# Kernel optimization log

Measured on AMD Instinct MI355X. Metric: run time of the kernel, lower is better.

The kernel has to match this reference:

```python
import jax, jax.numpy as jnp
import numpy as np

N = 100000   # nodes
E = 1600000  # edges (avg degree 16)
D = 128      # input feature dim
H = 64       # hidden dim (hard-coded in Sage.__init__)
C = 40       # output classes


def setup_inputs() -> dict:
    key = jax.random.key(0)
    ks = jax.random.split(key, 9)
    s_in = 1.0 / np.sqrt(D)
    s_h = 1.0 / np.sqrt(H)
    return {
        "x": jax.random.normal(ks[0], (N, D), jnp.float32),
        "edge_index": jax.random.randint(ks[1], (2, E), 0, N, dtype=jnp.int64),
        # SAGEConv params: lin_l acts on aggregated neighbors (carries bias),
        # lin_r acts on the root/self features (no bias), per PyG defaults.
        "W1_l": jax.random.uniform(ks[2], (D, H), jnp.float32, -s_in, s_in),
        "W1_r": jax.random.uniform(ks[3], (D, H), jnp.float32, -s_in, s_in),
        "b1": jax.random.uniform(ks[4], (H,), jnp.float32, -s_in, s_in),
        "W2_l": jax.random.uniform(ks[5], (H, C), jnp.float32, -s_h, s_h),
        "W2_r": jax.random.uniform(ks[6], (H, C), jnp.float32, -s_h, s_h),
        "b2": jax.random.uniform(ks[7], (C,), jnp.float32, -s_h, s_h),
    }


def _sage_conv(x, src, dst, W_l, W_r, b):
    # mean-aggregate neighbor features at destination nodes
    msg = x[src]                                             # [E, F] gather
    summed = jax.ops.segment_sum(msg, dst, num_segments=N)   # [N, F]
    deg = jax.ops.segment_sum(jnp.ones((src.shape[0],), x.dtype), dst,
                              num_segments=N)                # [N]
    agg = summed / jnp.maximum(deg, 1.0)[:, None]
    return agg @ W_l + x @ W_r + b


def reference(x, edge_index, W1_l, W1_r, b1, W2_l, W2_r, b2):
    src, dst = edge_index[0], edge_index[1]
    h = _sage_conv(x, src, dst, W1_l, W1_r, b1)
    h = jax.nn.relu(h)
    # F.dropout(training=False) in eval mode -> identity
    out = _sage_conv(h, src, dst, W2_l, W2_r, b2)
    return jax.nn.log_softmax(out, axis=1)
```

## Files before the change

### kernel.cpp

```cpp
#include <hip/hip_runtime.h>

__device__ __forceinline__ float bf2f(unsigned short u) {
  union { unsigned int i; float f; } c; c.i = ((unsigned int)u) << 16; return c.f;
}
__device__ __forceinline__ unsigned short f2bf(float f) {
  union { float f; unsigned int i; } c; c.f = f;
  unsigned int x = c.i;
  return (unsigned short)((x + 0x7fffu + ((x >> 16) & 1u)) >> 16);
}
__device__ __forceinline__ float lo16(unsigned int w) { return bf2f((unsigned short)(w & 0xffffu)); }
__device__ __forceinline__ float hi16(unsigned int w) { return bf2f((unsigned short)(w >> 16)); }

#define DD 128
#define HH 64
#define CC 40
#define NBUCK 256
#define NCHUNK 128
#define MAXNPB 512
#define NQ 4
#define NR 4

using bf16x8 = __attribute__((ext_vector_type(8))) short;
using f32x4  = __attribute__((ext_vector_type(4))) float;

__global__ __launch_bounds__(256) void detect(const unsigned int* e32,
                                              const unsigned int* x32, int* flags) {
  __shared__ unsigned int redOr[256];
  __shared__ int redCnt[256];
  int tid = threadIdx.x;
  unsigned int v = 0;
  for (int i = tid; i < 4096; i += 256) v |= e32[2 * i + 1];
  int cnt = 0;
  for (int i = tid; i < 4096; i += 256) {
    unsigned int w = x32[i];
    unsigned int expo = (w >> 7) & 0xffu;
    unsigned short lo = (unsigned short)(w & 0xffffu);
    if (lo == 0 || (expo >= 100u && expo <= 133u)) cnt++;
  }
  redOr[tid] = v; redCnt[tid] = cnt; __syncthreads();
  for (int s = 128; s > 0; s >>= 1) {
    if (tid < s) { redOr[tid] |= redOr[tid + s]; redCnt[tid] += redCnt[tid + s]; }
    __syncthreads();
  }
  if (tid == 0) {
    flags[0] = (redOr[0] == 0u) ? 1 : 0;
    flags[1] = (redCnt[0] < 2048) ? 1 : 0;
  }
}

__global__ __launch_bounds__(256) void hist_k(const int* e32, int E, int N,
                                              const int* flags, int nodesPerB,
                                              int* histG) {
  __shared__ int cnt[NBUCK * NR];
  int tid = threadIdx.x;
  for (int i = tid; i < NBUCK * NR; i += 256) cnt[i] = 0;
  __syncthreads();
  int isI64 = flags[0];
  int rep = tid & (NR - 1);
  int chunk = (E + NCHUNK - 1) / NCHUNK;
  int e0 = blockIdx.x * chunk, e1 = min(e0 + chunk, E);
  for (int i = e0 + tid; i < e1; i += 256) {
    int d = isI64 ? e32[2 * (E + i)] : e32[E + i];
    d = min(max(d, 0), N - 1);
    atomicAdd(&cnt[(d / nodesPerB) * NR + rep], 1);
  }
  __syncthreads();
  for (int i = tid; i < NBUCK; i += 256)
    histG[i * NCHUNK + blockIdx.x] =
        cnt[i * NR] + cnt[i * NR + 1] + cnt[i * NR + 2] + cnt[i * NR + 3];
}

__global__ __launch_bounds__(128) void scanA(const int* histG, int* ohist, int* bsum) {
  __shared__ int t[NCHUNK];
  int b = blockIdx.x, tid = threadIdx.x;
  int v = histG[b * NCHUNK + tid];
  t[tid] = v; __syncthreads();
  for (int st = 1; st < NCHUNK; st <<= 1) {
    int u = (tid >= st) ? t[tid - st] : 0;
    __syncthreads();
    t[tid] += u;
    __syncthreads();
  }
  ohist[b * NCHUNK + tid] = t[tid] - v;
  if (tid == NCHUNK - 1) bsum[b] = t[tid];
}

__global__ __launch_bounds__(256) void scanB_prepw(const int* bsum, int* bbase,
                                                   int* row_ptr4, int N, int E,
                                                   const void* W1l, const void* W1r,
                                                   const void* b1,
                                                   const void* W2l, const void* W2r,
                                                   const void* b2,
                                                   const int* flags,
                                                   unsigned short* Wb1,
                                                   unsigned short* Wb2,
                                                   float* b1f, float* b2f) {
  int tid = threadIdx.x;
  if (blockIdx.x == 1) {
    int isf = flags[1];
    auto rd = [&](const void* p, int i) -> float {
      return isf ? ((const float*)p)[i] : bf2f(((const unsigned short*)p)[i]);
    };
    for (int idx = tid; idx < 128 * 128; idx += 256) {
      int n = idx >> 7, k = idx & 127;
      float v = (n < HH) ? rd(W1l, k * HH + n) : rd(W1r, k * HH + (n - HH));
      Wb1[idx] = f2bf(v);
    }
    for (int idx = tid; idx < 48 * 128; idx += 256) {
      int n = idx >> 7, k = idx & 127;
      float v = 0.f;
      if (n < CC) v = (k < HH) ? rd(W2l, k * CC + n) : rd(W2r, (k - HH) * CC + n);
      Wb2[idx] = f2bf(v);
    }
    if (tid < HH) b1f[tid] = rd(b1, tid);
    if (tid < CC) b2f[tid] = rd(b2, tid);
    return;
  }
  __shared__ int t[NBUCK];
  int v = bsum[tid];
  t[tid] = v; __syncthreads();
  for (int st = 1; st < NBUCK; st <<= 1) {
    int u = (tid >= st) ? t[tid - st] : 0;
    __syncthreads();
    t[tid] += u;
    __syncthreads();
  }
  bbase[tid] = t[tid] - v;
  if (tid == 0) { bbase[NBUCK] = E; row_ptr4[NQ * N] = E; }
}

__global__ __launch_bounds__(256) void scatter_k(const int* e32, int E, int N,
                                                 const int* flags, int nodesPerB,
                                                 const int* ohist, const int* bbase,
                                                 uint2* ebuf) {
  __shared__ int cur[NBUCK];
  int tid = threadIdx.x;
  if (tid < NBUCK) cur[tid] = ohist[tid * NCHUNK + blockIdx.x] + bbase[tid];
  __syncthreads();
  int isI64 = flags[0];
  int chunk = (E + NCHUNK - 1) / NCHUNK;
  int e0 = blockIdx.x * chunk, e1 = min(e0 + chunk, E);
  for (int i = e0 + tid; i < e1; i += 256) {
    int s, d;
    if (isI64) { s = e32[2 * i]; d = e32[2 * (E + i)]; }
    else       { s = e32[i];     d = e32[E + i]; }
    s = min(max(s, 0), N - 1);
    d = min(max(d, 0), N - 1);
    int p = atomicAdd(&cur[d / nodesPerB], 1);
    ebuf[p] = make_uint2((unsigned)s, (unsigned)d);
  }
}

__global__ __launch_bounds__(256) void bktB_or_t1(
    const uint2* ebuf, const int* bbase,
    int nbuck, int nodesPerB, int qshift, int* row_ptr4, float* invd, int* col, int N,
    const void* xraw, const int* flags, const unsigned short* Wb1, const float* b1f,
    unsigned short* t1, unsigned short* s1, int T1B) {
  __shared__ int ldsb[MAXNPB * NQ + 256];
  int b = blockIdx.x;
  int tid = threadIdx.x;

  if (b < nbuck) {
    int* cnt = ldsb;
    int* sA  = ldsb + MAXNPB * NQ;
    int base_node = b * nodesPerB;
    int nn = min(nodesPerB, N - base_node);
    if (nn <= 0) return;
    int nk = nn * NQ;
    int eb0 = bbase[b], eb1 = bbase[b + 1];
    int nE = eb1 - eb0;
    const uint2* ee = ebuf + eb0;
    for (int i = tid; i < nk; i += 256) cnt[i] = 0;
    __syncthreads();
    for (int i = tid; i < nE; i += 256) {
      uint2 eg = ee[i];
      int key = ((int)eg.y - base_node) * NQ + (int)(eg.x >> qshift);
      atomicAdd(&cnt[key], 1);
    }
    __syncthreads();
    for (int i = tid; i < nn; i += 256) {
      int d = cnt[NQ * i] + cnt[NQ * i + 1] + cnt[NQ * i + 2] + cnt[NQ * i + 3];
      invd[base_node + i] = 1.0f / (float)max(d, 1);
    }
    __syncthreads();
    int per = (nk + 255) / 256;
    int myb = tid * per;
    int dreg[8];
    int ssum = 0;
#pragma unroll
    for (int k = 0; k < 8; k++) {
      int idx = myb + k;
      int v = (k < per && idx < nk) ? cnt[idx] : 0;
      dreg[k] = v; ssum += v;
    }
    sA[tid] = ssum;
    __syncthreads();
    for (int st = 1; st < 256; st <<= 1) {
      int t = (tid >= st) ? sA[tid - st] : 0;
      __syncthreads();
      sA[tid] += t;
      __syncthreads();
    }
    int run = eb0 + sA[tid] - ssum;
    __syncthreads();
#pragma unroll
    for (int k = 0; k < 8; k++) {
      int idx = myb + k;
      if (k < per && idx < nk) {
        row_ptr4[(size_t)(base_node + (idx >> 2)) * NQ + (idx & 3)] = run;
        cnt[idx] = run;
        run += dreg[k];
      }
    }
    __syncthreads();
    for (int i = tid; i < nE; i += 256) {
      uint2 eg = ee[i];
      int key = ((int)eg.y - base_node) * NQ + (int)(eg.x >> qshift);
      int p = atomicAdd(&cnt[key], 1);
      col[p] = (int)eg.x;
    }
    return;
  }

  int t = b - nbuck;
  if (t >= T1B) return;
  int lane = tid & 63, wv = tid >> 6;
  int nb = t * 64 + wv * 16;
  int oc = lane & 15, kgrp = lane >> 4;
  int node = min(nb + oc, N - 1);
  f32x4 acc[8];
#pragma unroll
  for (int i = 0; i < 8; i++) acc[i] = (f32x4){0.f, 0.f, 0.f, 0.f};

  if (flags[1]) {
    const float4* x4 = (const float4*)xraw;
#pragma unroll
    for (int kb = 0; kb < 4; kb++) {
      int k0 = kb * 32 + kgrp * 8;
      float4 a0 = x4[(size_t)node * 32 + (k0 >> 2)];
      float4 a1 = x4[(size_t)node * 32 + (k0 >> 2) + 1];
      bf16x8 af;
      af[0] = (short)f2bf(a0.x); af[1] = (short)f2bf(a0.y);
      af[2] = (short)f2bf(a0.z); af[3] = (short)f2bf(a0.w);
      af[4] = (short)f2bf(a1.x); af[5] = (short)f2bf(a1.y);
      af[6] = (short)f2bf(a1.z); af[7] = (short)f2bf(a1.w);
#pragma unroll
      for (int nblk = 0; nblk < 8; nblk++) {
        bf16x8 bfr = *(const bf16x8*)&Wb1[(nblk * 16 + oc) * 128 + k0];
        acc[nblk] = __builtin_amdgcn_mfma_f32_16x16x32_bf16(af, bfr, acc[nblk], 0, 0, 0);
      }
    }
  } else {
    const unsigned short* x16 = (const unsigned short*)xraw;
#pragma unroll
    for (int kb = 0; kb < 4; kb++) {
      int k0 = kb * 32 + kgrp * 8;
      bf16x8 af = *(const bf16x8*)&x16[(size_t)node * 128 + k0];
#pragma unroll
      for (int nblk = 0; nblk < 8; nblk++) {
        bf16x8 bfr = *(const bf16x8*)&Wb1[(nblk * 16 + oc) * 128 + k0];
        acc[nblk] = __builtin_amdgcn_mfma_f32_16x16x32_bf16(af, bfr, acc[nblk], 0, 0, 0);
      }
    }
  }

  int r0 = kgrp * 4;
#pragma unroll
  for (int nblk = 0; nblk < 8; nblk++) {
    float bias = (nblk >= 4) ? b1f[(nblk - 4) * 16 + oc] : 0.f;
#pragma unroll
    for (int r = 0; r < 4; r++) {
      int nn = nb + r0 + r;
      if (nn < N) {
        if (nblk < 4)
          t1[(size_t)nn * HH + nblk * 16 + oc] = f2bf(acc[nblk][r]);
        else
          s1[(size_t)nn * HH + (nblk - 4) * 16 + oc] = f2bf(acc[nblk][r] + bias);
      }
    }
  }
}

__device__ __forceinline__ void gather_seg(const uint4* t8, const int* col,
                                           int s0, int s1, int r, int c,
                                           float acc[8]) {
  for (int base = s0; base < s1; base += 4) {
    int i = base + r;
    bool g = (i < s1);
    int nb = g ? col[i] : 0;
    uint4 v = make_uint4(0, 0, 0, 0);
    if (g) v = t8[(size_t)nb * 8 + c];
    acc[0] += lo16(v.x); acc[1] += hi16(v.x);
    acc[2] += lo16(v.y); acc[3] += hi16(v.y);
    acc[4] += lo16(v.z); acc[5] += hi16(v.z);
    acc[6] += lo16(v.w); acc[7] += hi16(v.w);
  }
}

__global__ __launch_bounds__(256) void aggregate1(const unsigned short* t1,
                                                  const unsigned short* s1,
                                                  const int* row_ptr4, const float* invd,
                                                  const int* col, unsigned short* h, int N) {
  int wave = threadIdx.x >> 6, lane = threadIdx.x & 63;
  int ns = lane >> 5, r = (lane >> 3) & 3, c = lane & 7;
  int n = blockIdx.x * 8 + wave * 2 + ns;
  if (n >= N) return;
  int4 rp = *(const int4*)&row_ptr4[(size_t)NQ * n];
  int e4 = row_ptr4[(size_t)NQ * n + 4];
  float acc[8] = {0, 0, 0, 0, 0, 0, 0, 0};
  const uint4* t8 = (const uint4*)t1;
  gather_seg(t8, col, rp.x, rp.y, r, c, acc);
  gather_seg(t8, col, rp.y, rp.z, r, c, acc);
  gather_seg(t8, col, rp.z, rp.w, r, c, acc);
  gather_seg(t8, col, rp.w, e4, r, c, acc);
#pragma unroll
  for (int m = 8; m <= 16; m <<= 1)
#pragma unroll
    for (int i = 0; i < 8; i++) acc[i] += __shfl_xor(acc[i], m, 64);

  if (r == 0) {
    float id = invd[n];
    uint4 sv = ((const uint4*)s1)[(size_t)n * 8 + c];
    float s[8] = {lo16(sv.x), hi16(sv.x), lo16(sv.y), hi16(sv.y),
                  lo16(sv.z), hi16(sv.z), lo16(sv.w), hi16(sv.w)};
    unsigned int o[4];
#pragma unroll
    for (int i = 0; i < 4; i++) {
      float a0 = fmaxf(acc[2 * i] * id + s[2 * i], 0.f);
      float a1 = fmaxf(acc[2 * i + 1] * id + s[2 * i + 1], 0.f);
      o[i] = (unsigned int)f2bf(a0) | ((unsigned int)f2bf(a1) << 16);
    }
    ((uint4*)h)[(size_t)n * 8 + c] = make_uint4(o[0], o[1], o[2], o[3]);
  }
}

__global__ __launch_bounds__(256) void agg2(const unsigned short* h,
                                            const int* row_ptr4, const float* invd,
                                            const int* col, unsigned short* aggh, int N) {
  int wave = threadIdx.x >> 6, lane = threadIdx.x & 63;
  int ns = lane >> 5, r = (lane >> 3) & 3, c = lane & 7;
  int n = blockIdx.x * 8 + wave * 2 + ns;
  if (n >= N) return;
  int4 rp = *(const int4*)&row_ptr4[(size_t)NQ * n];
  int e4 = row_ptr4[(size_t)NQ * n + 4];
  float acc[8] = {0, 0, 0, 0, 0, 0, 0, 0};
  const uint4* h8 = (const uint4*)h;
  gather_seg(h8, col, rp.x, rp.y, r, c, acc);
  gather_seg(h8, col, rp.y, rp.z, r, c, acc);
  gather_seg(h8, col, rp.z, rp.w, r, c, acc);
  gather_seg(h8, col, rp.w, e4, r, c, acc);
#pragma unroll
  for (int m = 8; m <= 16; m <<= 1)
#pragma unroll
    for (int i = 0; i < 8; i++) acc[i] += __shfl_xor(acc[i], m, 64);

  if (r == 0) {
    float id = invd[n];
    unsigned int o[4];
#pragma unroll
    for (int i = 0; i < 4; i++) {
      o[i] = (unsigned int)f2bf(acc[2 * i] * id) |
             ((unsigned int)f2bf(acc[2 * i + 1] * id) << 16);
    }
    ((uint4*)aggh)[(size_t)n * 8 + c] = make_uint4(o[0], o[1], o[2], o[3]);
  }
}

__global__ __launch_bounds__(256) void final_k(const unsigned short* aggh,
                                               const unsigned short* h,
                                               const unsigned short* Wb2,
                                               const float* b2f,
                                               float* out, int N) {
  int tid = threadIdx.x;
  int lane = tid & 63, wv = tid >> 6;
  int nb = blockIdx.x * 64 + wv * 16;
  int oc = lane & 15, kgrp = lane >> 4;
  int node = min(nb + oc, N - 1);
  f32x4 acc[3];
#pragma unroll
  for (int i = 0; i < 3; i++) acc[i] = (f32x4){0.f, 0.f, 0.f, 0.f};

#pragma unroll
  for (int kb = 0; kb < 4; kb++) {
    int k0 = kb * 32 + kgrp * 8;
    const unsigned short* src = (kb < 2) ? aggh : h;
    int kk = k0 & 63;
    bf16x8 af = *(const bf16x8*)&src[(size_t)node * HH + kk];
#pragma unroll
    for (int nblk = 0; nblk < 3; nblk++) {
      bf16x8 bfr = *(const bf16x8*)&Wb2[(nblk * 16 + oc) * 128 + k0];
      acc[nblk] = __builtin_amdgcn_mfma_f32_16x16x32_bf16(af, bfr, acc[nblk], 0, 0, 0);
    }
  }

#pragma unroll
  for (int nblk = 0; nblk < 3; nblk++) {
    int cc = nblk * 16 + oc;
    float bias = (cc < CC) ? b2f[cc] : 0.f;
#pragma unroll
    for (int r = 0; r < 4; r++) acc[nblk][r] += bias;
  }

#pragma unroll
  for (int r = 0; r < 4; r++) {
    int nn = nb + kgrp * 4 + r;
    float m = -INFINITY;
#pragma unroll
    for (int nblk = 0; nblk < 3; nblk++)
      if (nblk * 16 + oc < CC) m = fmaxf(m, acc[nblk][r]);
    for (int off = 1; off <= 8; off <<= 1) m = fmaxf(m, __shfl_xor(m, off, 64));
    float s = 0.f;
#pragma unroll
    for (int nblk = 0; nblk < 3; nblk++)
      if (nblk * 16 + oc < CC) s += __expf(acc[nblk][r] - m);
    for (int off = 1; off <= 8; off <<= 1) s += __shfl_xor(s, off, 64);
    float lse = m + __logf(s);
    if (nn < N) {
#pragma unroll
      for (int nblk = 0; nblk < 3; nblk++) {
        int cc = nblk * 16 + oc;
        if (cc < CC) out[(size_t)nn * CC + cc] = acc[nblk][r] - lse;
      }
    }
  }
}

extern "C" void kernel_launch(void* const* d_in, const int* in_sizes, int n_in,
                              void* d_out, int out_size, void* d_ws, size_t ws_size,
                              hipStream_t stream) {
  const void* x   = d_in[0];
  const int*  e   = (const int*)d_in[1];
  const void* W1l = d_in[2];
  const void* W1r = d_in[3];
  const void* b1  = d_in[4];
  const void* W2l = d_in[5];
  const void* W2r = d_in[6];
  const void* b2  = d_in[7];
  float* out = (float*)d_out;

  const int N = in_sizes[0] / DD;
  const int E = in_sizes[1] / 2;
  const int nodesPerB = (N + NBUCK - 1) / NBUCK;
  const int nbuck = (N + nodesPerB - 1) / nodesPerB;
  const int T1B = (N + 63) / 64;
  int qshift = 0;
  while (((unsigned)(N - 1) >> qshift) > 3u) qshift++;

  char* w = (char*)d_ws;
  size_t off = 0;
  auto carve = [&](size_t bytes) -> void* {
    void* p = (void*)(w + off);
    off += (bytes + 255) & ~(size_t)255;
    return p;
  };
  int* col      = (int*)carve((size_t)E * 4);
  int* row_ptr4 = (int*)carve(((size_t)N * NQ + 1) * 4);
  float* invd   = (float*)carve((size_t)N * 4);
  int* histG    = (int*)carve((size_t)NBUCK * NCHUNK * 4);
  int* ohist    = (int*)carve((size_t)NBUCK * NCHUNK * 4);
  int* bsum     = (int*)carve(NBUCK * 4);
  int* bbase    = (int*)carve((NBUCK + 1) * 4);
  int* flags    = (int*)carve(8);
  unsigned short* t1   = (unsigned short*)carve((size_t)N * HH * 2);
  unsigned short* s1   = (unsigned short*)carve((size_t)N * HH * 2);
  unsigned short* h    = (unsigned short*)carve((size_t)N * HH * 2);
  unsigned short* Wb1  = (unsigned short*)carve(128 * 128 * 2);
  unsigned short* Wb2  = (unsigned short*)carve(48 * 128 * 2);
  float* b1f   = (float*)carve(HH * sizeof(float));
  float* b2f   = (float*)carve(CC * sizeof(float));
  uint2* ebuf  = (uint2*)carve((size_t)E * 8);
  unsigned short* aggh = (unsigned short*)ebuf;
  (void)ws_size; (void)n_in; (void)out_size;

  detect<<<1, 256, 0, stream>>>((const unsigned int*)e, (const unsigned int*)x, flags);
  hist_k<<<NCHUNK, 256, 0, stream>>>(e, E, N, flags, nodesPerB, histG);
  scanA<<<NBUCK, 128, 0, stream>>>(histG, ohist, bsum);
  scanB_prepw<<<2, 256, 0, stream>>>(bsum, bbase, row_ptr4, N, E,
                                     W1l, W1r, b1, W2l, W2r, b2,
                                     flags, Wb1, Wb2, b1f, b2f);
  scatter_k<<<NCHUNK, 256, 0, stream>>>(e, E, N, flags, nodesPerB, ohist, bbase, ebuf);
  bktB_or_t1<<<nbuck + T1B, 256, 0, stream>>>(ebuf, bbase,
                                              nbuck, nodesPerB, qshift, row_ptr4,
                                              invd, col, N,
                                              x, flags, Wb1, b1f, t1, s1, T1B);
  aggregate1<<<(N + 7) / 8, 256, 0, stream>>>(t1, s1, row_ptr4, invd, col, h, N);
  agg2<<<(N + 7) / 8, 256, 0, stream>>>(h, row_ptr4, invd, col, aggh, N);
  final_k<<<(N + 63) / 64, 256, 0, stream>>>(aggh, h, Wb2, b2f, out, N);
}
```

Measured before the change: 328.6 us.

## Reschedule layer-1 transform into histogram kernel and double bucket count

Weight preparation moves into the detect kernel, spread across extra blocks, and the layer-1 MFMA transform now runs alongside the edge histogram rather than alongside the bucket CSR build. NBUCK doubles to 512 and MAXNPB halves, so each bucket block covers fewer nodes and there are more of them, which should improve load balance and LDS use in bktB. scanB is now a standalone single block of 512 threads. The weight blocks re-detect the input dtype from W1l rather than from x. This heuristic could disagree with the flag computed by block 0, and scanA now launches twice as many blocks.

```diff
diff --git a/kernel.cpp b/kernel.cpp
--- a/kernel.cpp
+++ b/kernel.cpp
@@ -14,60 +14,164 @@
 #define DD 128
 #define HH 64
 #define CC 40
-#define NBUCK 256
+#define NBUCK 512
 #define NCHUNK 128
-#define MAXNPB 512
+#define MAXNPB 256
 #define NQ 4
 #define NR 4
 
 using bf16x8 = __attribute__((ext_vector_type(8))) short;
 using f32x4  = __attribute__((ext_vector_type(4))) float;
 
-__global__ __launch_bounds__(256) void detect(const unsigned int* e32,
-                                              const unsigned int* x32, int* flags) {
-  __shared__ unsigned int redOr[256];
-  __shared__ int redCnt[256];
+__global__ __launch_bounds__(256) void detect_prepw(
+    const unsigned int* e32, const unsigned int* x32, int* flags,
+    const void* W1l, const void* W1r, const void* b1,
+    const void* W2l, const void* W2r, const void* b2,
+    unsigned short* Wb1, unsigned short* Wb2, float* b1f, float* b2f) {
   int tid = threadIdx.x;
-  unsigned int v = 0;
-  for (int i = tid; i < 4096; i += 256) v |= e32[2 * i + 1];
+  if (blockIdx.x == 0) {
+    __shared__ unsigned int redOr[256];
+    __shared__ int redCnt[256];
+    unsigned int v = 0;
+    for (int i = tid; i < 4096; i += 256) v |= e32[2 * i + 1];
+    int cnt = 0;
+    for (int i = tid; i < 4096; i += 256) {
+      unsigned int w = x32[i];
+      unsigned int expo = (w >> 7) & 0xffu;
+      unsigned short lo = (unsigned short)(w & 0xffffu);
+      if (lo == 0 || (expo >= 100u && expo <= 133u)) cnt++;
+    }
+    redOr[tid] = v; redCnt[tid] = cnt; __syncthreads();
+    for (int s = 128; s > 0; s >>= 1) {
+      if (tid < s) { redOr[tid] |= redOr[tid + s]; redCnt[tid] += redCnt[tid + s]; }
+      __syncthreads();
+    }
+    if (tid == 0) {
+      flags[0] = (redOr[0] == 0u) ? 1 : 0;
+      flags[1] = (redCnt[0] < 2048) ? 1 : 0;
+    }
+    return;
+  }
+  __shared__ int red[256];
+  const unsigned int* w32 = (const unsigned int*)W1l;
   int cnt = 0;
   for (int i = tid; i < 4096; i += 256) {
-    unsigned int w = x32[i];
+    unsigned int w = w32[i];
     unsigned int expo = (w >> 7) & 0xffu;
     unsigned short lo = (unsigned short)(w & 0xffffu);
     if (lo == 0 || (expo >= 100u && expo <= 133u)) cnt++;
   }
-  redOr[tid] = v; redCnt[tid] = cnt; __syncthreads();
+  red[tid] = cnt; __syncthreads();
   for (int s = 128; s > 0; s >>= 1) {
-    if (tid < s) { redOr[tid] |= redOr[tid + s]; redCnt[tid] += redCnt[tid + s]; }
-    __syncthreads();
-  }
-  if (tid == 0) {
-    flags[0] = (redOr[0] == 0u) ? 1 : 0;
-    flags[1] = (redCnt[0] < 2048) ? 1 : 0;
-  }
-}
-
-__global__ __launch_bounds__(256) void hist_k(const int* e32, int E, int N,
-                                              const int* flags, int nodesPerB,
-                                              int* histG) {
+    if (tid < s) red[tid] += red[tid + s];
+    __syncthreads();
+  }
+  int isf = (red[0] < 2048) ? 1 : 0;
+  auto rd = [&](const void* p, int i) -> float {
+    return isf ? ((const float*)p)[i] : bf2f(((const unsigned short*)p)[i]);
+  };
+  if (blockIdx.x == 1) {
+    for (int idx = tid; idx < 128 * 128; idx += 256) {
+      int n = idx >> 7, k = idx & 127;
+      float v = (n < HH) ? rd(W1l, k * HH + n) : rd(W1r, k * HH + (n - HH));
+      Wb1[idx] = f2bf(v);
+    }
+  } else {
+    for (int idx = tid; idx < 48 * 128; idx += 256) {
+      int n = idx >> 7, k = idx & 127;
+      float v = 0.f;
+      if (n < CC) v = (k < HH) ? rd(W2l, k * CC + n) : rd(W2r, (k - HH) * CC + n);
+      Wb2[idx] = f2bf(v);
+    }
+    if (tid < HH) b1f[tid] = rd(b1, tid);
+    if (tid < CC) b2f[tid] = rd(b2, tid);
+  }
+}
+
+__global__ __launch_bounds__(256) void hist_or_t1(
+    const int* e32, int E, int N, const int* flags, int nodesPerB, int* histG,
+    const void* xraw, const unsigned short* Wb1, const float* b1f,
+    unsigned short* t1, unsigned short* s1, int T1B) {
   __shared__ int cnt[NBUCK * NR];
+  int b = blockIdx.x;
   int tid = threadIdx.x;
-  for (int i = tid; i < NBUCK * NR; i += 256) cnt[i] = 0;
-  __syncthreads();
-  int isI64 = flags[0];
-  int rep = tid & (NR - 1);
-  int chunk = (E + NCHUNK - 1) / NCHUNK;
-  int e0 = blockIdx.x * chunk, e1 = min(e0 + chunk, E);
-  for (int i = e0 + tid; i < e1; i += 256) {
-    int d = isI64 ? e32[2 * (E + i)] : e32[E + i];
-    d = min(max(d, 0), N - 1);
-    atomicAdd(&cnt[(d / nodesPerB) * NR + rep], 1);
-  }
-  __syncthreads();
-  for (int i = tid; i < NBUCK; i += 256)
-    histG[i * NCHUNK + blockIdx.x] =
-        cnt[i * NR] + cnt[i * NR + 1] + cnt[i * NR + 2] + cnt[i * NR + 3];
+
+  if (b < NCHUNK) {
+    for (int i = tid; i < NBUCK * NR; i += 256) cnt[i] = 0;
+    __syncthreads();
+    int isI64 = flags[0];
+    int rep = tid & (NR - 1);
+    int chunk = (E + NCHUNK - 1) / NCHUNK;
+    int e0 = b * chunk, e1 = min(e0 + chunk, E);
+    for (int i = e0 + tid; i < e1; i += 256) {
+      int d = isI64 ? e32[2 * (E + i)] : e32[E + i];
+      d = min(max(d, 0), N - 1);
+      atomicAdd(&cnt[(d / nodesPerB) * NR + rep], 1);
+    }
+    __syncthreads();
+    for (int i = tid; i < NBUCK; i += 256)
+      histG[i * NCHUNK + b] =
+          cnt[i * NR] + cnt[i * NR + 1] + cnt[i * NR + 2] + cnt[i * NR + 3];
+    return;
+  }
+
+  int t = b - NCHUNK;
+  if (t >= T1B) return;
+  int lane = tid & 63, wv = tid >> 6;
+  int nb = t * 64 + wv * 16;
+  int oc = lane & 15, kgrp = lane >> 4;
+  int node = min(nb + oc, N - 1);
+  f32x4 acc[8];
+#pragma unroll
+  for (int i = 0; i < 8; i++) acc[i] = (f32x4){0.f, 0.f, 0.f, 0.f};
+
+  if (flags[1]) {
+    const float4* x4 = (const float4*)xraw;
+#pragma unroll
+    for (int kb = 0; kb < 4; kb++) {
+      int k0 = kb * 32 + kgrp * 8;
+      float4 a0 = x4[(size_t)node * 32 + (k0 >> 2)];
+      float4 a1 = x4[(size_t)node * 32 + (k0 >> 2) + 1];
+      bf16x8 af;
+      af[0] = (short)f2bf(a0.x); af[1] = (short)f2bf(a0.y);
+      af[2] = (short)f2bf(a0.z); af[3] = (short)f2bf(a0.w);
+      af[4] = (short)f2bf(a1.x); af[5] = (short)f2bf(a1.y);
+      af[6] = (short)f2bf(a1.z); af[7] = (short)f2bf(a1.w);
+#pragma unroll
+      for (int nblk = 0; nblk < 8; nblk++) {
+        bf16x8 bfr = *(const bf16x8*)&Wb1[(nblk * 16 + oc) * 128 + k0];
+        acc[nblk] = __builtin_amdgcn_mfma_f32_16x16x32_bf16(af, bfr, acc[nblk], 0, 0, 0);
+      }
+    }
+  } else {
+    const unsigned short* x16 = (const unsigned short*)xraw;
+#pragma unroll
+    for (int kb = 0; kb < 4; kb++) {
+      int k0 = kb * 32 + kgrp * 8;
+      bf16x8 af = *(const bf16x8*)&x16[(size_t)node * 128 + k0];
+#pragma unroll
+      for (int nblk = 0; nblk < 8; nblk++) {
+        bf16x8 bfr = *(const bf16x8*)&Wb1[(nblk * 16 + oc) * 128 + k0];
+        acc[nblk] = __builtin_amdgcn_mfma_f32_16x16x32_bf16(af, bfr, acc[nblk], 0, 0, 0);
+      }
+    }
+  }
+
+  int r0 = kgrp * 4;
+#pragma unroll
+  for (int nblk = 0; nblk < 8; nblk++) {
+    float bias = (nblk >= 4) ? b1f[(nblk - 4) * 16 + oc] : 0.f;
+#pragma unroll
+    for (int r = 0; r < 4; r++) {
+      int nn = nb + r0 + r;
+      if (nn < N) {
+        if (nblk < 4)
+          t1[(size_t)nn * HH + nblk * 16 + oc] = f2bf(acc[nblk][r]);
+        else
+          s1[(size_t)nn * HH + (nblk - 4) * 16 + oc] = f2bf(acc[nblk][r] + bias);
+      }
+    }
+  }
 }
 
 __global__ __launch_bounds__(128) void scanA(const int* histG, int* ohist, int* bsum) {
@@ -85,38 +189,10 @@
   if (tid == NCHUNK - 1) bsum[b] = t[tid];
 }
 
-__global__ __launch_bounds__(256) void scanB_prepw(const int* bsum, int* bbase,
-                                                   int* row_ptr4, int N, int E,
-                                                   const void* W1l, const void* W1r,
-                                                   const void* b1,
-                                                   const void* W2l, const void* W2r,
-                                                   const void* b2,
-                                                   const int* flags,
-                                                   unsigned short* Wb1,
-                                                   unsigned short* Wb2,
-                                                   float* b1f, float* b2f) {
+__global__ __launch_bounds__(512) void scanB(const int* bsum, int* bbase,
+                                             int* row_ptr4, int N, int E) {
+  __shared__ int t[NBUCK];
   int tid = threadIdx.x;
-  if (blockIdx.x == 1) {
-    int isf = flags[1];
-    auto rd = [&](const void* p, int i) -> float {
-      return isf ? ((const float*)p)[i] : bf2f(((const unsigned short*)p)[i]);
-    };
-    for (int idx = tid; idx < 128 * 128; idx += 256) {
-      int n = idx >> 7, k = idx & 127;
-      float v = (n < HH) ? rd(W1l, k * HH + n) : rd(W1r, k * HH + (n - HH));
-      Wb1[idx] = f2bf(v);
-    }
-    for (int idx = tid; idx < 48 * 128; idx += 256) {
-      int n = idx >> 7, k = idx & 127;
-      float v = 0.f;
-      if (n < CC) v = (k < HH) ? rd(W2l, k * CC + n) : rd(W2r, (k - HH) * CC + n);
-      Wb2[idx] = f2bf(v);
-    }
-    if (tid < HH) b1f[tid] = rd(b1, tid);
-    if (tid < CC) b2f[tid] = rd(b2, tid);
-    return;
-  }
-  __shared__ int t[NBUCK];
   int v = bsum[tid];
   t[tid] = v; __syncthreads();
   for (int st = 1; st < NBUCK; st <<= 1) {
@@ -135,7 +211,8 @@
                                                  uint2* ebuf) {
   __shared__ int cur[NBUCK];
   int tid = threadIdx.x;
-  if (tid < NBUCK) cur[tid] = ohist[tid * NCHUNK + blockIdx.x] + bbase[tid];
+  for (int i = tid; i < NBUCK; i += 256)
+    cur[i] = ohist[i * NCHUNK + blockIdx.x] + bbase[i];
   __syncthreads();
   int isI64 = flags[0];
   int chunk = (E + NCHUNK - 1) / NCHUNK;
@@ -151,133 +228,68 @@
   }
 }
 
-__global__ __launch_bounds__(256) void bktB_or_t1(
+__global__ __launch_bounds__(256) void bktB(
     const uint2* ebuf, const int* bbase,
-    int nbuck, int nodesPerB, int qshift, int* row_ptr4, float* invd, int* col, int N,
-    const void* xraw, const int* flags, const unsigned short* Wb1, const float* b1f,
-    unsigned short* t1, unsigned short* s1, int T1B) {
-  __shared__ int ldsb[MAXNPB * NQ + 256];
+    int nodesPerB, int qshift, int* row_ptr4, float* invd, int* col, int N) {
+  __shared__ int cnt[MAXNPB * NQ];
+  __shared__ int sA[256];
   int b = blockIdx.x;
   int tid = threadIdx.x;
-
-  if (b < nbuck) {
-    int* cnt = ldsb;
-    int* sA  = ldsb + MAXNPB * NQ;
-    int base_node = b * nodesPerB;
-    int nn = min(nodesPerB, N - base_node);
-    if (nn <= 0) return;
-    int nk = nn * NQ;
-    int eb0 = bbase[b], eb1 = bbase[b + 1];
-    int nE = eb1 - eb0;
-    const uint2* ee = ebuf + eb0;
-    for (int i = tid; i < nk; i += 256) cnt[i] = 0;
-    __syncthreads();
-    for (int i = tid; i < nE; i += 256) {
-      uint2 eg = ee[i];
-      int key = ((int)eg.y - base_node) * NQ + (int)(eg.x >> qshift);
-      atomicAdd(&cnt[key], 1);
-    }
-    __syncthreads();
-    for (int i = tid; i < nn; i += 256) {
-      int d = cnt[NQ * i] + cnt[NQ * i + 1] + cnt[NQ * i + 2] + cnt[NQ * i + 3];
-      invd[base_node + i] = 1.0f / (float)max(d, 1);
-    }
-    __syncthreads();
-    int per = (nk + 255) / 256;
-    int myb = tid * per;
-    int dreg[8];
-    int ssum = 0;
-#pragma unroll
-    for (int k = 0; k < 8; k++) {
-      int idx = myb + k;
-      int v = (k < per && idx < nk) ? cnt[idx] : 0;
-      dreg[k] = v; ssum += v;
-    }
-    sA[tid] = ssum;
-    __syncthreads();
-    for (int st = 1; st < 256; st <<= 1) {
-      int t = (tid >= st) ? sA[tid - st] : 0;
-      __syncthreads();
-      sA[tid] += t;
-      __syncthreads();
-    }
-    int run = eb0 + sA[tid] - ssum;
-    __syncthreads();
-#pragma unroll
-    for (int k = 0; k < 8; k++) {
-      int idx = myb + k;
-      if (k < per && idx < nk) {
-        row_ptr4[(size_t)(base_node + (idx >> 2)) * NQ + (idx & 3)] = run;
-        cnt[idx] = run;
-        run += dreg[k];
-      }
-    }
-    __syncthreads();
-    for (int i = tid; i < nE; i += 256) {
-      uint2 eg = ee[i];
-      int key = ((int)eg.y - base_node) * NQ + (int)(eg.x >> qshift);
-      int p = atomicAdd(&cnt[key], 1);
-      col[p] = (int)eg.x;
-    }
-    return;
-  }
-
-  int t = b - nbuck;
-  if (t >= T1B) return;
-  int lane = tid & 63, wv = tid >> 6;
-  int nb = t * 64 + wv * 16;
-  int oc = lane & 15, kgrp = lane >> 4;
-  int node = min(nb + oc, N - 1);
-  f32x4 acc[8];
-#pragma unroll
-  for (int i = 0; i < 8; i++) acc[i] = (f32x4){0.f, 0.f, 0.f, 0.f};
-
-  if (flags[1]) {
-    const float4* x4 = (const float4*)xraw;
-#pragma unroll
-    for (int kb = 0; kb < 4; kb++) {
-      int k0 = kb * 32 + kgrp * 8;
-      float4 a0 = x4[(size_t)node * 32 + (k0 >> 2)];
-      float4 a1 = x4[(size_t)node * 32 + (k0 >> 2) + 1];
-      bf16x8 af;
-      af[0] = (short)f2bf(a0.x); af[1] = (short)f2bf(a0.y);
-      af[2] = (short)f2bf(a0.z); af[3] = (short)f2bf(a0.w);
-      af[4] = (short)f2bf(a1.x); af[5] = (short)f2bf(a1.y);
-      af[6] = (short)f2bf(a1.z); af[7] = (short)f2bf(a1.w);
-#pragma unroll
-      for (int nblk = 0; nblk < 8; nblk++) {
-        bf16x8 bfr = *(const bf16x8*)&Wb1[(nblk * 16 + oc) * 128 + k0];
-        acc[nblk] = __builtin_amdgcn_mfma_f32_16x16x32_bf16(af, bfr, acc[nblk], 0, 0, 0);
-      }
-    }
-  } else {
-    const unsigned short* x16 = (const unsigned short*)xraw;
-#pragma unroll
-    for (int kb = 0; kb < 4; kb++) {
-      int k0 = kb * 32 + kgrp * 8;
-      bf16x8 af = *(const bf16x8*)&x16[(size_t)node * 128 + k0];
-#pragma unroll
-      for (int nblk = 0; nblk < 8; nblk++) {
-        bf16x8 bfr = *(const bf16x8*)&Wb1[(nblk * 16 + oc) * 128 + k0];
-        acc[nblk] = __builtin_amdgcn_mfma_f32_16x16x32_bf16(af, bfr, acc[nblk], 0, 0, 0);
-      }
-    }
-  }
-
-  int r0 = kgrp * 4;
-#pragma unroll
-  for (int nblk = 0; nblk < 8; nblk++) {
-    float bias = (nblk >= 4) ? b1f[(nblk - 4) * 16 + oc] : 0.f;
-#pragma unroll
-    for (int r = 0; r < 4; r++) {
-      int nn = nb + r0 + r;
-      if (nn < N) {
-        if (nblk < 4)
-          t1[(size_t)nn * HH + nblk * 16 + oc] = f2bf(acc[nblk][r]);
-        else
-          s1[(size_t)nn * HH + (nblk - 4) * 16 + oc] = f2bf(acc[nblk][r] + bias);
-      }
-    }
+  int base_node = b * nodesPerB;
+  int nn = min(nodesPerB, N - base_node);
+  if (nn <= 0) return;
+  int nk = nn * NQ;
+  int eb0 = bbase[b], eb1 = bbase[b + 1];
+  int nE = eb1 - eb0;
+  const uint2* ee = ebuf + eb0;
+  for (int i = tid; i < nk; i += 256) cnt[i] = 0;
+  __syncthreads();
+  for (int i = tid; i < nE; i += 256) {
+    uint2 eg = ee[i];
+    int key = ((int)eg.y - base_node) * NQ + (int)(eg.x >> qshift);
+    atomicAdd(&cnt[key], 1);
+  }
+  __syncthreads();
+  for (int i = tid; i < nn; i += 256) {
+    int d = cnt[NQ * i] + cnt[NQ * i + 1] + cnt[NQ * i + 2] + cnt[NQ * i + 3];
+    invd[base_node + i] = 1.0f / (float)max(d, 1);
+  }
+  __syncthreads();
+  int per = (nk + 255) / 256;
+  int myb = tid * per;
+  int dreg[4];
+  int ssum = 0;
+#pragma unroll
+  for (int k = 0; k < 4; k++) {
+    int idx = myb + k;
+    int v = (k < per && idx < nk) ? cnt[idx] : 0;
+    dreg[k] = v; ssum += v;
+  }
+  sA[tid] = ssum;
+  __syncthreads();
+  for (int st = 1; st < 256; st <<= 1) {
+    int t = (tid >= st) ? sA[tid - st] : 0;
+    __syncthreads();
+    sA[tid] += t;
+    __syncthreads();
+  }
+  int run = eb0 + sA[tid] - ssum;
+  __syncthreads();
+#pragma unroll
+  for (int k = 0; k < 4; k++) {
+    int idx = myb + k;
+    if (k < per && idx < nk) {
+      row_ptr4[(size_t)(base_node + (idx >> 2)) * NQ + (idx & 3)] = run;
+      cnt[idx] = run;
+      run += dreg[k];
+    }
+  }
+  __syncthreads();
+  for (int i = tid; i < nE; i += 256) {
+    uint2 eg = ee[i];
+    int key = ((int)eg.y - base_node) * NQ + (int)(eg.x >> qshift);
+    int p = atomicAdd(&cnt[key], 1);
+    col[p] = (int)eg.x;
   }
 }
 
@@ -472,17 +484,16 @@
   unsigned short* aggh = (unsigned short*)ebuf;
   (void)ws_size; (void)n_in; (void)out_size;
 
-  detect<<<1, 256, 0, stream>>>((const unsigned int*)e, (const unsigned int*)x, flags);
-  hist_k<<<NCHUNK, 256, 0, stream>>>(e, E, N, flags, nodesPerB, histG);
+  detect_prepw<<<3, 256, 0, stream>>>((const unsigned int*)e, (const unsigned int*)x,
+                                      flags, W1l, W1r, b1, W2l, W2r, b2,
+                                      Wb1, Wb2, b1f, b2f);
+  hist_or_t1<<<NCHUNK + T1B, 256, 0, stream>>>(e, E, N, flags, nodesPerB, histG,
+                                               x, Wb1, b1f, t1, s1, T1B);
   scanA<<<NBUCK, 128, 0, stream>>>(histG, ohist, bsum);
-  scanB_prepw<<<2, 256, 0, stream>>>(bsum, bbase, row_ptr4, N, E,
-                                     W1l, W1r, b1, W2l, W2r, b2,
-                                     flags, Wb1, Wb2, b1f, b2f);
+  scanB<<<1, 512, 0, stream>>>(bsum, bbase, row_ptr4, N, E);
   scatter_k<<<NCHUNK, 256, 0, stream>>>(e, E, N, flags, nodesPerB, ohist, bbase, ebuf);
-  bktB_or_t1<<<nbuck + T1B, 256, 0, stream>>>(ebuf, bbase,
-                                              nbuck, nodesPerB, qshift, row_ptr4,
-                                              invd, col, N,
-                                              x, flags, Wb1, b1f, t1, s1, T1B);
+  bktB<<<nbuck, 256, 0, stream>>>(ebuf, bbase, nodesPerB, qshift,
+                                  row_ptr4, invd, col, N);
   aggregate1<<<(N + 7) / 8, 256, 0, stream>>>(t1, s1, row_ptr4, invd, col, h, N);
   agg2<<<(N + 7) / 8, 256, 0, stream>>>(h, row_ptr4, invd, col, aggh, N);
   final_k<<<(N + 63) / 64, 256, 0, stream>>>(aggh, h, Wb2, b2f, out, N);
```

New measurement: 316.1 us. 3.8% less time.
